# Kernel tuning notes

Hardware: AMD Instinct MI355X
Metric: run time of the kernel (lower is better)

Reference implementation:

```python
import jax, jax.numpy as jnp
import numpy as np
from jax import lax

B, EMB, HEADS, HD, LAYERS, FIX, ADAPT, MLP, NCLS = 32, 768, 12, 64, 12, 6, 6, 3072, 100
PE_N, PE_D = 100, 256
SCALE = 1.0 / np.sqrt(HD)


def _ln(x, g, b, eps=1e-5):
    m = jnp.mean(x, axis=-1, keepdims=True)
    v = jnp.mean((x - m) ** 2, axis=-1, keepdims=True)
    return (x - m) / jnp.sqrt(v + eps) * g + b


def _vit_block(x, g1, b1, qkvw, qkvb, pw, pb, g2, b2, f1w, f1b, f2w, f2b):
    Bn, N, _ = x.shape
    h = _ln(x, g1, b1)
    qkv = (h @ qkvw + qkvb).reshape(Bn, N, 3, HEADS, HD)
    q, k, v = [qkv[:, :, i].transpose(0, 2, 1, 3) for i in range(3)]  # [B,H,N,hd]
    attn = jax.nn.softmax(jnp.einsum('bhqd,bhkd->bhqk', q, k) * SCALE, axis=-1)
    o = jnp.einsum('bhqk,bhkd->bhqd', attn, v).transpose(0, 2, 1, 3).reshape(Bn, N, EMB)
    x = x + (o @ pw + pb)
    h = _ln(x, g2, b2)
    return x + (jax.nn.gelu(h @ f1w + f1b, approximate=False) @ f2w + f2b)


def _sinusoid_table():
    pos = np.arange(PE_N)[:, None].astype(np.float64)
    j = np.arange(PE_D)[None, :]
    ang = pos / np.power(10000.0, 2 * (j // 2) / PE_D)
    tab = ang.copy()
    tab[:, 0::2] = np.sin(ang[:, 0::2])
    tab[:, 1::2] = np.cos(ang[:, 1::2])
    return jnp.asarray(tab, dtype=jnp.float32)


def setup_inputs() -> dict:
    key = jax.random.key(0)
    ks = iter(jax.random.split(key, 40))
    r = lambda shape: jax.random.normal(next(ks), shape, dtype=jnp.float32) * 0.02
    inp = {
        'x': jax.random.normal(next(ks), (B, 3, 224, 224), dtype=jnp.float32),
        'budget': jax.random.uniform(next(ks), (B,), dtype=jnp.float32),
        'pe_table': _sinusoid_table(),
        'lat_w1': r((PE_D, EMB)), 'lat_b1': r((EMB,)),
        'lat_ln_g': jnp.ones((EMB,), jnp.float32), 'lat_ln_b': jnp.zeros((EMB,), jnp.float32),
        'lat_w2': r((EMB, EMB)), 'lat_b2': r((EMB,)),
        'patch_w': r((EMB, 3, 16, 16)), 'patch_b': r((EMB,)),
        'cls_token': r((1, 1, EMB)), 'pos_embed': r((1, 198, EMB)),
        'sched_w': r((EMB, ADAPT)), 'sched_b': r((ADAPT,)),
        'ln1_g': jnp.ones((LAYERS, EMB), jnp.float32), 'ln1_b': jnp.zeros((LAYERS, EMB), jnp.float32),
        'qkv_w': r((LAYERS, EMB, 3 * EMB)), 'qkv_b': r((LAYERS, 3 * EMB)),
        'proj_w': r((LAYERS, EMB, EMB)), 'proj_b': r((LAYERS, EMB)),
        'ln2_g': jnp.ones((LAYERS, EMB), jnp.float32), 'ln2_b': jnp.zeros((LAYERS, EMB), jnp.float32),
        'fc1_w': r((LAYERS, EMB, MLP)), 'fc1_b': r((LAYERS, MLP)),
        'fc2_w': r((LAYERS, MLP, EMB)), 'fc2_b': r((LAYERS, EMB)),
        'norm_g': jnp.ones((EMB,), jnp.float32), 'norm_b': jnp.zeros((EMB,), jnp.float32),
        'head_w': r((EMB, NCLS)), 'head_b': r((NCLS,)),
    }
    return inp


def reference(x, budget, pe_table, lat_w1, lat_b1, lat_ln_g, lat_ln_b, lat_w2, lat_b2,
              patch_w, patch_b, cls_token, pos_embed, sched_w, sched_b,
              ln1_g, ln1_b, qkv_w, qkv_b, proj_w, proj_b, ln2_g, ln2_b,
              fc1_w, fc1_b, fc2_w, fc2_b, norm_g, norm_b, head_w, head_b):
    Bn = x.shape[0]
    bud = lax.stop_gradient(budget)
    # latency encoder
    idx = jnp.round(bud * (PE_N - 1)).astype(jnp.int32)
    h = pe_table[idx] @ lat_w1 + lat_b1
    h = jax.nn.gelu(h, approximate=False)
    h = _ln(h, lat_ln_g, lat_ln_b)
    lat = (h @ lat_w2 + lat_b2)[:, None, :]  # [B,1,EMB]
    # patch embed: conv16 s16 -> [B,EMB,14,14]
    p = lax.conv_general_dilated(x, patch_w, (16, 16), 'VALID',
                                 dimension_numbers=('NCHW', 'OIHW', 'NCHW'))
    p = (p + patch_b[None, :, None, None]).reshape(Bn, EMB, 196).transpose(0, 2, 1)
    tok = jnp.concatenate([lat, jnp.broadcast_to(cls_token, (Bn, 1, EMB)), p], axis=1)
    tok = tok + pos_embed  # [B,198,EMB]
    blk = lambda t, i: _vit_block(t, ln1_g[i], ln1_b[i], qkv_w[i], qkv_b[i], proj_w[i], proj_b[i],
                                  ln2_g[i], ln2_b[i], fc1_w[i], fc1_b[i], fc2_w[i], fc2_b[i])
    for i in range(FIX):
        tok = blk(tok, i)
    # layer routing (eval path): per-sample top-k over adaptive layers
    logits = tok[:, 0] @ sched_w + sched_b  # [B,ADAPT]
    k = jnp.maximum(jnp.ceil(bud * ADAPT).astype(jnp.int32), 1)  # [B]
    ranks = jnp.argsort(jnp.argsort(-logits, axis=-1), axis=-1)
    active = ranks < k[:, None]  # [B,ADAPT] bool
    t = tok[:, 1:]  # drop latency token -> [B,197,EMB]
    for i in range(ADAPT):
        out = blk(t, FIX + i)
        t = jnp.where(active[:, i, None, None], out, t)
    t = _ln(t, norm_g, norm_b)
    return t[:, 0] @ head_w + head_b
```

## Files before the change

kernel.cpp:

```cpp
#include <hip/hip_runtime.h>
#include <hip/hip_bf16.h>
#include <math.h>


using bf16   = __hip_bfloat16;
using short8 = __attribute__((ext_vector_type(8))) short;
using f32x4  = __attribute__((ext_vector_type(4))) float;

#define GLD16(gptr, lptr)                                                            \
    __builtin_amdgcn_global_load_lds((const __attribute__((address_space(1))) void*)(gptr), \
                                     (__attribute__((address_space(3))) void*)(lptr), 16, 0, 0)

__device__ __forceinline__ void split2(float x, short& h, short& l)
{
    unsigned u  = __float_as_uint(x);
    unsigned hr = (u + 0x7fffu + ((u >> 16) & 1u)) & 0xffff0000u;
    h = (short)(hr >> 16);
    float res = x - __uint_as_float(hr);
    l = (short)(__float_as_uint(res) >> 16);
}

__global__ __launch_bounds__(256) void trans_split_kernel(const float* __restrict__ W,
                                                          short* __restrict__ Wh,
                                                          short* __restrict__ Wl,
                                                          int K, int N)
{
    __shared__ float tile[32][33];
    int n0 = blockIdx.x * 32, k0 = blockIdx.y * 32;
    int c = threadIdx.x & 31, r = threadIdx.x >> 5;
    #pragma unroll
    for (int i = 0; i < 32; i += 8)
        tile[r + i][c] = W[(size_t)(k0 + r + i) * N + n0 + c];
    __syncthreads();
    #pragma unroll
    for (int i = 0; i < 32; i += 8) {
        short h, l; split2(tile[c][r + i], h, l);
        size_t o = (size_t)(n0 + r + i) * K + k0 + c;
        Wh[o] = h; Wl[o] = l;
    }
}

__global__ void split_kernel(const float* __restrict__ in, short* __restrict__ h,
                             short* __restrict__ l, int n)
{
    int i = blockIdx.x * 256 + threadIdx.x;
    if (i >= n) return;
    short hh, ll; split2(in[i], hh, ll);
    h[i] = hh; l[i] = ll;
}

__global__ void im2col_split_kernel(const float* __restrict__ x,
                                    short* __restrict__ Ah, short* __restrict__ Al)
{
    int idx = blockIdx.x * 256 + threadIdx.x;
    if (idx >= 6272 * 768) return;
    int k = idx % 768;
    int row = idx / 768;
    int b = row / 196, p = row % 196;
    int py = p / 14, px = p % 14;
    int c = k >> 8, rem = k & 255;
    int i = rem >> 4, j = rem & 15;
    float v = x[(((size_t)b * 3 + c) * 224 + py * 16 + i) * 224 + px * 16 + j];
    short h, l; split2(v, h, l);
    Ah[idx] = h; Al[idx] = l;
}

template<bool GELU, bool RES, bool SPLITOUT>
__global__ __launch_bounds__(256) void gemm3_kernel(const short* __restrict__ Ah,
                                                    const short* __restrict__ Al,
                                                    const short* __restrict__ Bh,
                                                    const short* __restrict__ Bl,
                                                    const float* __restrict__ bias,
                                                    const float* __restrict__ resid,
                                                    float* __restrict__ Cf,
                                                    short* __restrict__ Ch,
                                                    short* __restrict__ Cl,
                                                    int M, int N, int K)
{
    __shared__ __align__(16) short Ash[128 * 32];
    __shared__ __align__(16) short Asl[128 * 32];
    __shared__ __align__(16) short Bsh[128 * 32];
    __shared__ __align__(16) short Bsl[128 * 32];
    const int tid  = threadIdx.x;
    const int lane = tid & 63;
    const int w    = tid >> 6;
    const int wm   = w >> 1, wn = w & 1;
    const int m0   = blockIdx.y * 128;
    const int n0   = blockIdx.x * 128;
    const int col  = lane & 15;
    const int quad = lane >> 4;
    const int srow = lane >> 2;
    const int skc  = (lane & 3) * 8;

    f32x4 acc[4][4];
    #pragma unroll
    for (int i = 0; i < 4; ++i)
        #pragma unroll
        for (int j = 0; j < 4; ++j) acc[i][j] = (f32x4)0.f;

    const short* Ahb = Ah + (size_t)m0 * K;
    const short* Alb = Al + (size_t)m0 * K;
    const short* Bhb = Bh + (size_t)n0 * K;
    const short* Blb = Bl + (size_t)n0 * K;

    for (int k0 = 0; k0 < K; k0 += 32) {
        #pragma unroll
        for (int i = 0; i < 2; ++i) {
            int r = w * 32 + i * 16;
            size_t go = (size_t)(r + srow) * K + k0 + skc;
            GLD16(Ahb + go, &Ash[r * 32]);
            GLD16(Alb + go, &Asl[r * 32]);
            GLD16(Bhb + go, &Bsh[r * 32]);
            GLD16(Blb + go, &Bsl[r * 32]);
        }
        __syncthreads();
        short8 ah[4], al[4];
        #pragma unroll
        for (int mi = 0; mi < 4; ++mi) {
            int ao = (wm * 64 + mi * 16 + col) * 32 + quad * 8;
            ah[mi] = *(const short8*)&Ash[ao];
            al[mi] = *(const short8*)&Asl[ao];
        }
        #pragma unroll
        for (int ni = 0; ni < 4; ++ni) {
            int bo = (wn * 64 + ni * 16 + col) * 32 + quad * 8;
            short8 bh = *(const short8*)&Bsh[bo];
            short8 bl = *(const short8*)&Bsl[bo];
            #pragma unroll
            for (int mi = 0; mi < 4; ++mi) {
                acc[mi][ni] = __builtin_amdgcn_mfma_f32_16x16x32_bf16(ah[mi], bh, acc[mi][ni], 0, 0, 0);
                acc[mi][ni] = __builtin_amdgcn_mfma_f32_16x16x32_bf16(al[mi], bh, acc[mi][ni], 0, 0, 0);
                acc[mi][ni] = __builtin_amdgcn_mfma_f32_16x16x32_bf16(ah[mi], bl, acc[mi][ni], 0, 0, 0);
            }
        }
        __syncthreads();
    }

    #pragma unroll
    for (int mi = 0; mi < 4; ++mi) {
        #pragma unroll
        for (int ni = 0; ni < 4; ++ni) {
            int gcol = n0 + wn * 64 + ni * 16 + col;
            float bv = bias[gcol];
            #pragma unroll
            for (int r = 0; r < 4; ++r) {
                int grow = m0 + wm * 64 + mi * 16 + quad * 4 + r;
                if (grow < M) {
                    float v = acc[mi][ni][r] + bv;
                    if (RES) v += resid[(size_t)grow * N + gcol];
                    if (GELU) v = 0.5f * v * (1.f + erff(v * 0.70710678118654752f));
                    size_t o = (size_t)grow * N + gcol;
                    if (SPLITOUT) { short h, l; split2(v, h, l); Ch[o] = h; Cl[o] = l; }
                    else          Cf[o] = v;
                }
            }
        }
    }
}

__global__ __launch_bounds__(256) void ln_kernel(const float* __restrict__ x,
                                                 const float* __restrict__ g,
                                                 const float* __restrict__ bta,
                                                 short* __restrict__ outh,
                                                 short* __restrict__ outl, int M)
{
    int row = blockIdx.x * 4 + (threadIdx.x >> 6);
    int lane = threadIdx.x & 63;
    if (row >= M) return;
    const float* xr = x + (size_t)row * 768;
    float vals[12];
    float s = 0.f;
    #pragma unroll
    for (int i = 0; i < 12; ++i) { vals[i] = xr[lane + i * 64]; s += vals[i]; }
    #pragma unroll
    for (int off = 32; off; off >>= 1) s += __shfl_xor(s, off);
    float mean = s * (1.f / 768.f);
    float vs = 0.f;
    #pragma unroll
    for (int i = 0; i < 12; ++i) { float d = vals[i] - mean; vs += d * d; }
    #pragma unroll
    for (int off = 32; off; off >>= 1) vs += __shfl_xor(vs, off);
    float rstd = rsqrtf(vs * (1.f / 768.f) + 1e-5f);
    size_t rb = (size_t)row * 768;
    #pragma unroll
    for (int i = 0; i < 12; ++i) {
        int c = lane + i * 64;
        short h, l; split2((vals[i] - mean) * rstd * g[c] + bta[c], h, l);
        outh[rb + c] = h; outl[rb + c] = l;
    }
}

__global__ __launch_bounds__(256) void attn_kernel(const float* __restrict__ qkv,
                                                   short* __restrict__ Oh,
                                                   short* __restrict__ Ol, int S)
{
    __shared__ float Ks[128 * 64];
    __shared__ float Vs[128 * 64];
    int bh = blockIdx.x;
    int b = bh / 12, h = bh % 12;
    const float* base = qkv + (size_t)b * S * 2304;
    int tid = threadIdx.x;
    int r = tid;
    bool act = (r < S);
    float q[64];
    #pragma unroll
    for (int d = 0; d < 64; ++d) q[d] = 0.f;
    if (act) {
        const float4* qp = (const float4*)(base + (size_t)r * 2304 + h * 64);
        #pragma unroll
        for (int d4 = 0; d4 < 16; ++d4) {
            float4 t = qp[d4];
            q[4 * d4] = t.x; q[4 * d4 + 1] = t.y; q[4 * d4 + 2] = t.z; q[4 * d4 + 3] = t.w;
        }
    }
    float o[64];
    #pragma unroll
    for (int d = 0; d < 64; ++d) o[d] = 0.f;
    float m = -1e30f, l = 0.f;

    for (int jc = 0; jc < S; jc += 128) {
        int cnt = min(128, S - jc);
        __syncthreads();
        for (int idx = tid; idx < cnt * 64; idx += 256) {
            int j = idx >> 6, d = idx & 63;
            const float* rp = base + (size_t)(jc + j) * 2304 + h * 64 + d;
            Ks[idx] = rp[768];
            Vs[idx] = rp[1536];
        }
        __syncthreads();
        if (act) {
            for (int j = 0; j < cnt; ++j) {
                const float4* kr = (const float4*)&Ks[j * 64];
                float s0 = 0.f, s1 = 0.f, s2 = 0.f, s3 = 0.f;
                #pragma unroll
                for (int d4 = 0; d4 < 16; ++d4) {
                    float4 kv = kr[d4];
                    s0 += q[4 * d4]     * kv.x;
                    s1 += q[4 * d4 + 1] * kv.y;
                    s2 += q[4 * d4 + 2] * kv.z;
                    s3 += q[4 * d4 + 3] * kv.w;
                }
                float s = ((s0 + s1) + (s2 + s3)) * 0.125f;
                float mn = fmaxf(m, s);
                float alpha = expf(m - mn);
                float p = expf(s - mn);
                l = l * alpha + p;
                m = mn;
                const float4* vr = (const float4*)&Vs[j * 64];
                #pragma unroll
                for (int d4 = 0; d4 < 16; ++d4) {
                    float4 vv = vr[d4];
                    o[4 * d4]     = o[4 * d4]     * alpha + p * vv.x;
                    o[4 * d4 + 1] = o[4 * d4 + 1] * alpha + p * vv.y;
                    o[4 * d4 + 2] = o[4 * d4 + 2] * alpha + p * vv.z;
                    o[4 * d4 + 3] = o[4 * d4 + 3] * alpha + p * vv.w;
                }
            }
        }
    }
    if (act) {
        float inv = 1.f / l;
        size_t rb = (size_t)(b * S + r) * 768 + h * 64;
        #pragma unroll
        for (int d = 0; d < 64; ++d) {
            short hh, ll; split2(o[d] * inv, hh, ll);
            Oh[rb + d] = hh; Ol[rb + d] = ll;
        }
    }
}

__global__ __launch_bounds__(256) void latent_kernel(const float* __restrict__ pe_table,
                                                     const float* __restrict__ budget,
                                                     const float* __restrict__ w1, const float* __restrict__ b1,
                                                     const float* __restrict__ lng, const float* __restrict__ lnb,
                                                     const float* __restrict__ w2, const float* __restrict__ b2,
                                                     float* __restrict__ lat)
{
    int b = blockIdx.x, tid = threadIdx.x;
    __shared__ float pe[256];
    __shared__ float hbuf[768];
    __shared__ float red[256];
    int idx = (int)rintf(budget[b] * 99.f);
    pe[tid] = pe_table[idx * 256 + tid];
    __syncthreads();
    float hv[3];
    #pragma unroll
    for (int t = 0; t < 3; ++t) {
        int colc = tid + t * 256;
        float a = b1[colc];
        for (int k = 0; k < 256; ++k) a += pe[k] * w1[k * 768 + colc];
        hv[t] = 0.5f * a * (1.f + erff(a * 0.70710678118654752f));
    }
    float s = hv[0] + hv[1] + hv[2];
    red[tid] = s; __syncthreads();
    for (int o = 128; o > 0; o >>= 1) { if (tid < o) red[tid] += red[tid + o]; __syncthreads(); }
    float mean = red[0] * (1.f / 768.f);
    __syncthreads();
    float vs = 0.f;
    #pragma unroll
    for (int t = 0; t < 3; ++t) { float d = hv[t] - mean; vs += d * d; }
    red[tid] = vs; __syncthreads();
    for (int o = 128; o > 0; o >>= 1) { if (tid < o) red[tid] += red[tid + o]; __syncthreads(); }
    float rstd = rsqrtf(red[0] * (1.f / 768.f) + 1e-5f);
    __syncthreads();
    #pragma unroll
    for (int t = 0; t < 3; ++t) {
        int colc = tid + t * 256;
        hbuf[colc] = (hv[t] - mean) * rstd * lng[colc] + lnb[colc];
    }
    __syncthreads();
    #pragma unroll
    for (int t = 0; t < 3; ++t) {
        int colc = tid + t * 256;
        float a = b2[colc];
        for (int k = 0; k < 768; ++k) a += hbuf[k] * w2[k * 768 + colc];
        lat[b * 768 + colc] = a;
    }
}

__global__ void assemble_kernel(const float* __restrict__ lat, const float* __restrict__ cls,
                                const float* __restrict__ P, const float* __restrict__ pos,
                                float* __restrict__ T)
{
    int idx = blockIdx.x * 256 + threadIdx.x;
    if (idx >= 32 * 198 * 768) return;
    int c = idx % 768;
    int row = idx / 768;
    int b = row / 198, t = row % 198;
    float v;
    if (t == 0)      v = lat[b * 768 + c];
    else if (t == 1) v = cls[c];
    else             v = P[((size_t)b * 196 + (t - 2)) * 768 + c];
    T[idx] = v + pos[t * 768 + c];
}

__global__ void sched_kernel(const float* __restrict__ T, const float* __restrict__ sw,
                             const float* __restrict__ sb, const float* __restrict__ budget,
                             int* __restrict__ active)
{
    int b = blockIdx.x, lane = threadIdx.x;
    const float* xr = T + (size_t)b * 198 * 768;
    float acc[6] = {0, 0, 0, 0, 0, 0};
    for (int k = lane; k < 768; k += 64) {
        float xv = xr[k];
        #pragma unroll
        for (int i = 0; i < 6; ++i) acc[i] += xv * sw[k * 6 + i];
    }
    #pragma unroll
    for (int i = 0; i < 6; ++i)
        #pragma unroll
        for (int off = 32; off; off >>= 1) acc[i] += __shfl_xor(acc[i], off);
    if (lane == 0) {
        float lg[6];
        #pragma unroll
        for (int i = 0; i < 6; ++i) lg[i] = acc[i] + sb[i];
        int k = (int)ceilf(budget[b] * 6.f);
        if (k < 1) k = 1;
        for (int i = 0; i < 6; ++i) {
            int rank = 0;
            for (int j = 0; j < 6; ++j)
                rank += (lg[j] > lg[i]) || (lg[j] == lg[i] && j < i);
            active[b * 6 + i] = (rank < k) ? 1 : 0;
        }
    }
}

__global__ void droplat_kernel(const float* __restrict__ T, float* __restrict__ T2)
{
    int idx = blockIdx.x * 256 + threadIdx.x;
    if (idx >= 32 * 197 * 768) return;
    int c = idx % 768;
    int row = idx / 768;
    int b = row / 197, t = row % 197;
    T2[idx] = T[((size_t)b * 198 + t + 1) * 768 + c];
}

__global__ void select_kernel(float* __restrict__ T2, const float* __restrict__ OUT,
                              const int* __restrict__ active, int layer)
{
    int idx = blockIdx.x * 256 + threadIdx.x;
    if (idx >= 32 * 197 * 768) return;
    int b = idx / (197 * 768);
    if (active[b * 6 + layer]) T2[idx] = OUT[idx];
}

__global__ __launch_bounds__(128) void head_kernel(const float* __restrict__ T2,
                                                   const float* __restrict__ g,
                                                   const float* __restrict__ bta,
                                                   const float* __restrict__ hw,
                                                   const float* __restrict__ hb,
                                                   float* __restrict__ out)
{
    int b = blockIdx.x, tid = threadIdx.x;
    __shared__ float hn[768];
    __shared__ float red[128];
    const float* xr = T2 + (size_t)b * 197 * 768;
    float v[6];
    float s = 0.f;
    #pragma unroll
    for (int i = 0; i < 6; ++i) { v[i] = xr[tid + i * 128]; s += v[i]; }
    red[tid] = s; __syncthreads();
    for (int o = 64; o > 0; o >>= 1) { if (tid < o) red[tid] += red[tid + o]; __syncthreads(); }
    float mean = red[0] * (1.f / 768.f);
    __syncthreads();
    float vs = 0.f;
    #pragma unroll
    for (int i = 0; i < 6; ++i) { float d = v[i] - mean; vs += d * d; }
    red[tid] = vs; __syncthreads();
    for (int o = 64; o > 0; o >>= 1) { if (tid < o) red[tid] += red[tid + o]; __syncthreads(); }
    float rstd = rsqrtf(red[0] * (1.f / 768.f) + 1e-5f);
    #pragma unroll
    for (int i = 0; i < 6; ++i) {
        int c = tid + i * 128;
        hn[c] = (v[i] - mean) * rstd * g[c] + bta[c];
    }
    __syncthreads();
    if (tid < 100) {
        float a = hb[tid];
        for (int k = 0; k < 768; ++k) a += hn[k] * hw[k * 100 + tid];
        out[b * 100 + tid] = a;
    }
}

extern "C" void kernel_launch(void* const* d_in, const int* in_sizes, int n_in,
                              void* d_out, int out_size, void* d_ws, size_t ws_size,
                              hipStream_t stream)
{
    const float* x        = (const float*)d_in[0];
    const float* budget   = (const float*)d_in[1];
    const float* pe_table = (const float*)d_in[2];
    const float* lat_w1   = (const float*)d_in[3];
    const float* lat_b1   = (const float*)d_in[4];
    const float* lat_ln_g = (const float*)d_in[5];
    const float* lat_ln_b = (const float*)d_in[6];
    const float* lat_w2   = (const float*)d_in[7];
    const float* lat_b2   = (const float*)d_in[8];
    const float* patch_w  = (const float*)d_in[9];
    const float* patch_b  = (const float*)d_in[10];
    const float* cls_tok  = (const float*)d_in[11];
    const float* pos_emb  = (const float*)d_in[12];
    const float* sched_w  = (const float*)d_in[13];
    const float* sched_b  = (const float*)d_in[14];
    const float* ln1_g    = (const float*)d_in[15];
    const float* ln1_b    = (const float*)d_in[16];
    const float* qkv_w    = (const float*)d_in[17];
    const float* qkv_b    = (const float*)d_in[18];
    const float* proj_w   = (const float*)d_in[19];
    const float* proj_b   = (const float*)d_in[20];
    const float* ln2_g    = (const float*)d_in[21];
    const float* ln2_b    = (const float*)d_in[22];
    const float* fc1_w    = (const float*)d_in[23];
    const float* fc1_b    = (const float*)d_in[24];
    const float* fc2_w    = (const float*)d_in[25];
    const float* fc2_b    = (const float*)d_in[26];
    const float* norm_g   = (const float*)d_in[27];
    const float* norm_b   = (const float*)d_in[28];
    const float* head_w   = (const float*)d_in[29];
    const float* head_b   = (const float*)d_in[30];
    float* out = (float*)d_out;
    (void)in_sizes; (void)n_in; (void)out_size; (void)ws_size;

    char* ws = (char*)d_ws;
    size_t off = 0;
    auto alloc = [&](size_t bytes) -> char* {
        char* p = ws + off;
        off = (off + bytes + 255) & ~(size_t)255;
        return p;
    };
    short* sQKVh = (short*)alloc(2304ull * 768 * 2);
    short* sQKVl = (short*)alloc(2304ull * 768 * 2);
    short* sPRJh = (short*)alloc(768ull * 768 * 2);
    short* sPRJl = (short*)alloc(768ull * 768 * 2);
    short* sFC1h = (short*)alloc(3072ull * 768 * 2);
    short* sFC1l = (short*)alloc(3072ull * 768 * 2);
    short* sFC2h = (short*)alloc(768ull * 3072 * 2);
    short* sFC2l = (short*)alloc(768ull * 3072 * 2);
    short* pwh   = (short*)alloc(768ull * 768 * 2);
    short* pwl   = (short*)alloc(768ull * 768 * 2);
    float* T     = (float*)alloc(6400ull * 768 * 4);
    float* T2    = (float*)alloc(6400ull * 768 * 4);
    float* OUT   = (float*)alloc(6400ull * 768 * 4);
    short* Hh    = (short*)alloc(6400ull * 768 * 2);
    short* Hl    = (short*)alloc(6400ull * 768 * 2);
    float* QKV   = (float*)alloc(6336ull * 2304 * 4);
    short* Oh    = (short*)alloc(6400ull * 768 * 2);
    short* Ol    = (short*)alloc(6400ull * 768 * 2);
    short* Mh    = (short*)alloc(6400ull * 3072 * 2);
    short* Ml    = (short*)alloc(6400ull * 3072 * 2);
    float* lat   = (float*)alloc(32ull * 768 * 4);
    int*   act   = (int*)alloc(32 * 6 * 4);
    float* P     = QKV;
    short* Aph   = Mh;
    short* Apl   = Ml;

    im2col_split_kernel<<<(6272 * 768 + 255) / 256, 256, 0, stream>>>(x, Aph, Apl);
    split_kernel<<<(768 * 768 + 255) / 256, 256, 0, stream>>>(patch_w, pwh, pwl, 768 * 768);
    latent_kernel<<<32, 256, 0, stream>>>(pe_table, budget, lat_w1, lat_b1,
                                          lat_ln_g, lat_ln_b, lat_w2, lat_b2, lat);
    gemm3_kernel<false, false, false><<<dim3(6, 49), 256, 0, stream>>>(
        Aph, Apl, pwh, pwl, patch_b, nullptr, P, nullptr, nullptr, 6272, 768, 768);
    assemble_kernel<<<(32 * 198 * 768 + 255) / 256, 256, 0, stream>>>(lat, cls_tok, P, pos_emb, T);

    for (int l = 0; l < 6; ++l) {
        trans_split_kernel<<<dim3(72, 24), 256, 0, stream>>>(qkv_w + (size_t)l * 768 * 2304, sQKVh, sQKVl, 768, 2304);
        trans_split_kernel<<<dim3(24, 24), 256, 0, stream>>>(proj_w + (size_t)l * 768 * 768, sPRJh, sPRJl, 768, 768);
        trans_split_kernel<<<dim3(96, 24), 256, 0, stream>>>(fc1_w + (size_t)l * 768 * 3072, sFC1h, sFC1l, 768, 3072);
        trans_split_kernel<<<dim3(24, 96), 256, 0, stream>>>(fc2_w + (size_t)l * 3072 * 768, sFC2h, sFC2l, 3072, 768);

        ln_kernel<<<6336 / 4, 256, 0, stream>>>(T, ln1_g + l * 768, ln1_b + l * 768, Hh, Hl, 6336);
        gemm3_kernel<false, false, false><<<dim3(18, 50), 256, 0, stream>>>(
            Hh, Hl, sQKVh, sQKVl, qkv_b + l * 2304, nullptr, QKV, nullptr, nullptr, 6336, 2304, 768);
        attn_kernel<<<384, 256, 0, stream>>>(QKV, Oh, Ol, 198);
        gemm3_kernel<false, true, false><<<dim3(6, 50), 256, 0, stream>>>(
            Oh, Ol, sPRJh, sPRJl, proj_b + l * 768, T, T, nullptr, nullptr, 6336, 768, 768);
        ln_kernel<<<6336 / 4, 256, 0, stream>>>(T, ln2_g + l * 768, ln2_b + l * 768, Hh, Hl, 6336);
        gemm3_kernel<true, false, true><<<dim3(24, 50), 256, 0, stream>>>(
            Hh, Hl, sFC1h, sFC1l, fc1_b + l * 3072, nullptr, nullptr, Mh, Ml, 6336, 3072, 768);
        gemm3_kernel<false, true, false><<<dim3(6, 50), 256, 0, stream>>>(
            Mh, Ml, sFC2h, sFC2l, fc2_b + l * 768, T, T, nullptr, nullptr, 6336, 768, 3072);
    }

    sched_kernel<<<32, 64, 0, stream>>>(T, sched_w, sched_b, budget, act);
    droplat_kernel<<<(32 * 197 * 768 + 255) / 256, 256, 0, stream>>>(T, T2);

    for (int i = 0; i < 6; ++i) {
        int l = 6 + i;
        trans_split_kernel<<<dim3(72, 24), 256, 0, stream>>>(qkv_w + (size_t)l * 768 * 2304, sQKVh, sQKVl, 768, 2304);
        trans_split_kernel<<<dim3(24, 24), 256, 0, stream>>>(proj_w + (size_t)l * 768 * 768, sPRJh, sPRJl, 768, 768);
        trans_split_kernel<<<dim3(96, 24), 256, 0, stream>>>(fc1_w + (size_t)l * 768 * 3072, sFC1h, sFC1l, 768, 3072);
        trans_split_kernel<<<dim3(24, 96), 256, 0, stream>>>(fc2_w + (size_t)l * 3072 * 768, sFC2h, sFC2l, 3072, 768);

        ln_kernel<<<6304 / 4, 256, 0, stream>>>(T2, ln1_g + l * 768, ln1_b + l * 768, Hh, Hl, 6304);
        gemm3_kernel<false, false, false><<<dim3(18, 50), 256, 0, stream>>>(
            Hh, Hl, sQKVh, sQKVl, qkv_b + l * 2304, nullptr, QKV, nullptr, nullptr, 6304, 2304, 768);
        attn_kernel<<<384, 256, 0, stream>>>(QKV, Oh, Ol, 197);
        gemm3_kernel<false, true, false><<<dim3(6, 50), 256, 0, stream>>>(
            Oh, Ol, sPRJh, sPRJl, proj_b + l * 768, T2, OUT, nullptr, nullptr, 6304, 768, 768);
        ln_kernel<<<6304 / 4, 256, 0, stream>>>(OUT, ln2_g + l * 768, ln2_b + l * 768, Hh, Hl, 6304);
        gemm3_kernel<true, false, true><<<dim3(24, 50), 256, 0, stream>>>(
            Hh, Hl, sFC1h, sFC1l, fc1_b + l * 3072, nullptr, nullptr, Mh, Ml, 6304, 3072, 768);
        gemm3_kernel<false, true, false><<<dim3(6, 50), 256, 0, stream>>>(
            Mh, Ml, sFC2h, sFC2l, fc2_b + l * 768, OUT, OUT, nullptr, nullptr, 6304, 768, 3072);
        select_kernel<<<(32 * 197 * 768 + 255) / 256, 256, 0, stream>>>(T2, OUT, act, i);
    }

    head_kernel<<<32, 128, 0, stream>>>(T2, norm_g, norm_b, head_w, head_b, out);
}
```

Measured before the change: 8.426 ms.

## Double-buffer GEMM LDS tiles and XOR-swizzle layout to avoid bank conflicts

Merges the four shared tiles into one buffer with two stages, so the global-to-LDS loads for the next K slice are issued before computing on the current one. This removes one barrier per iteration. It also applies an XOR swizzle to the 16-byte chunk placement in LDS, applied on both write and read, to reduce bank conflicts on the MFMA operand reads. Shared memory per block doubles, which may reduce occupancy.

```diff
diff --git a/kernel.cpp b/kernel.cpp
--- a/kernel.cpp
+++ b/kernel.cpp
@@ -77,10 +77,7 @@
                                                     short* __restrict__ Cl,
                                                     int M, int N, int K)
 {
-    __shared__ __align__(16) short Ash[128 * 32];
-    __shared__ __align__(16) short Asl[128 * 32];
-    __shared__ __align__(16) short Bsh[128 * 32];
-    __shared__ __align__(16) short Bsl[128 * 32];
+    __shared__ __align__(16) short sm[2 * 4 * 128 * 32];
     const int tid  = threadIdx.x;
     const int lane = tid & 63;
     const int w    = tid >> 6;
@@ -90,7 +87,8 @@
     const int col  = lane & 15;
     const int quad = lane >> 4;
     const int srow = lane >> 2;
-    const int skc  = (lane & 3) * 8;
+    const int skc  = (((lane & 3) ^ ((lane >> 3) & 3)) * 8);
+    const int rswz = (quad ^ ((col >> 1) & 3)) * 8;
 
     f32x4 acc[4][4];
     #pragma unroll
@@ -103,29 +101,34 @@
     const short* Bhb = Bh + (size_t)n0 * K;
     const short* Blb = Bl + (size_t)n0 * K;
 
-    for (int k0 = 0; k0 < K; k0 += 32) {
+    auto stage = [&](int buf, int t) {
+        const int k0 = t << 5;
+        short* dst = &sm[buf * 16384];
         #pragma unroll
         for (int i = 0; i < 2; ++i) {
             int r = w * 32 + i * 16;
             size_t go = (size_t)(r + srow) * K + k0 + skc;
-            GLD16(Ahb + go, &Ash[r * 32]);
-            GLD16(Alb + go, &Asl[r * 32]);
-            GLD16(Bhb + go, &Bsh[r * 32]);
-            GLD16(Blb + go, &Bsl[r * 32]);
-        }
-        __syncthreads();
+            GLD16(Ahb + go, dst + r * 32);
+            GLD16(Alb + go, dst + 4096 + r * 32);
+            GLD16(Bhb + go, dst + 8192 + r * 32);
+            GLD16(Blb + go, dst + 12288 + r * 32);
+        }
+    };
+
+    auto compute = [&](int buf) {
+        const short* cb = &sm[buf * 16384];
         short8 ah[4], al[4];
         #pragma unroll
         for (int mi = 0; mi < 4; ++mi) {
-            int ao = (wm * 64 + mi * 16 + col) * 32 + quad * 8;
-            ah[mi] = *(const short8*)&Ash[ao];
-            al[mi] = *(const short8*)&Asl[ao];
+            int ao = (wm * 64 + mi * 16 + col) * 32 + rswz;
+            ah[mi] = *(const short8*)(cb + ao);
+            al[mi] = *(const short8*)(cb + 4096 + ao);
         }
         #pragma unroll
         for (int ni = 0; ni < 4; ++ni) {
-            int bo = (wn * 64 + ni * 16 + col) * 32 + quad * 8;
-            short8 bh = *(const short8*)&Bsh[bo];
-            short8 bl = *(const short8*)&Bsl[bo];
+            int bo = (wn * 64 + ni * 16 + col) * 32 + rswz;
+            short8 bh = *(const short8*)(cb + 8192 + bo);
+            short8 bl = *(const short8*)(cb + 12288 + bo);
             #pragma unroll
             for (int mi = 0; mi < 4; ++mi) {
                 acc[mi][ni] = __builtin_amdgcn_mfma_f32_16x16x32_bf16(ah[mi], bh, acc[mi][ni], 0, 0, 0);
@@ -133,8 +136,19 @@
                 acc[mi][ni] = __builtin_amdgcn_mfma_f32_16x16x32_bf16(ah[mi], bl, acc[mi][ni], 0, 0, 0);
             }
         }
+    };
+
+    const int nk = K >> 5;
+    stage(0, 0);
+    __syncthreads();
+    int cur = 0;
+    for (int t = 0; t < nk - 1; ++t) {
+        stage(cur ^ 1, t + 1);
+        compute(cur);
         __syncthreads();
-    }
+        cur ^= 1;
+    }
+    compute(cur);
 
     #pragma unroll
     for (int mi = 0; mi < 4; ++mi) {
```

Result: faster. 7.758 ms (-7.9%).
